# Performance work log

Hardware: AMD Instinct MI355X
Metric: run time of the kernel (lower is better)

## Reference

```python
import jax, jax.numpy as jnp
import numpy as np

V, E, H2, B, T, OUT = 50000, 300, 512, 32, 512, 256
H = H2 // 2  # hidden per direction


def _rand_mask(key, lengths, n_true):
    # exactly n_true True positions per row, all within the valid prefix [0, len)
    t = jnp.arange(T)[None, :]
    r = jax.random.uniform(key, (B, T)) + (t >= lengths[:, None]) * 10.0
    idx = jnp.argsort(r, axis=1)[:, :n_true]
    mask = jnp.zeros((B, T), dtype=bool)
    return mask.at[jnp.arange(B)[:, None], idx].set(True)


def setup_inputs() -> dict:
    key = jax.random.key(0)
    ks = jax.random.split(key, 12)
    inputs = jax.random.randint(ks[0], (B, T), 0, V)
    lengths = jnp.sort(jax.random.randint(ks[1], (B,), OUT, T + 1))[::-1]
    lengths = lengths.at[0].set(T)  # max length == padded length
    fmask = _rand_mask(ks[2], lengths, OUT)
    bmask = _rand_mask(ks[3], lengths, OUT)
    emb_scale = np.sqrt(3.0 / E).astype(np.float32)
    emb = jax.random.uniform(ks[4], (V, E), minval=-emb_scale, maxval=emb_scale, dtype=jnp.float32)
    k = 1.0 / np.sqrt(H).astype(np.float32)
    def u(kk, shape):
        return jax.random.uniform(kk, shape, minval=-k, maxval=k, dtype=jnp.float32)
    return {
        'inputs': inputs, 'seq_length': lengths, 'fmask': fmask, 'bmask': bmask,
        'out_seq_length': OUT, 'emb': emb,
        'W_ih_f': u(ks[5], (4 * H, E)), 'W_hh_f': u(ks[6], (4 * H, H)),
        'b_ih_f': u(ks[7], (4 * H,)), 'b_hh_f': u(ks[8], (4 * H,)),
        'W_ih_b': u(ks[9], (4 * H, E)), 'W_hh_b': u(ks[10], (4 * H, H)),
        'b_ih_b': u(ks[11], (4 * H,)), 'b_hh_b': u(ks[7], (4 * H,)),
    }


def run_lstm(xe, W_ih, W_hh, b_ih, b_hh):
    # PyTorch LSTM cell, gate order i,f,g,o. xe: (B,T,E) -> (B,T,H)
    xg = jnp.einsum('bte,ge->btg', xe, W_ih) + (b_ih + b_hh)
    def step(carry, xg_t):
        h, c = carry
        g = xg_t + h @ W_hh.T
        i, f, gg, o = jnp.split(g, 4, axis=-1)
        c = jax.nn.sigmoid(f) * c + jax.nn.sigmoid(i) * jnp.tanh(gg)
        h = jax.nn.sigmoid(o) * jnp.tanh(c)
        return (h, c), h
    h0 = jnp.zeros((xe.shape[0], W_hh.shape[1]), xe.dtype)
    _, hs = jax.lax.scan(step, (h0, h0), xg.transpose(1, 0, 2))
    return hs.transpose(1, 0, 2)


def select_masked(x, mask, out_len):
    # masked_select row-major order == indices of True in increasing t
    idx = jnp.argsort(jnp.logical_not(mask), axis=1, stable=True)[:, :out_len]
    return jnp.take_along_axis(x, idx[:, :, None], axis=1)


def reference(inputs, seq_length, fmask, bmask, out_seq_length, emb,
              W_ih_f, W_hh_f, b_ih_f, b_hh_f, W_ih_b, W_hh_b, b_ih_b, b_hh_b):
    t = jnp.arange(inputs.shape[1])[None, :]          # (1,T)
    valid = t < seq_length[:, None]                   # (B,T)
    # forward direction (dropout is identity at inference)
    f_out = run_lstm(emb[inputs], W_ih_f, W_hh_f, b_ih_f, b_hh_f)
    f_out = f_out * valid[..., None]                  # pad_packed zeros beyond len
    fsel = select_masked(f_out, fmask, out_seq_length)
    # per-batch sequence reversal of valid prefix (padding stays in place)
    rev_idx = jnp.where(valid, seq_length[:, None] - 1 - t, t)
    rinputs = jnp.take_along_axis(inputs, rev_idx, axis=1)
    b_out = run_lstm(emb[rinputs], W_ih_b, W_hh_b, b_ih_b, b_hh_b)
    b_out = b_out * valid[..., None]
    bsel = select_masked(b_out, bmask, out_seq_length)
    # re-reverse selected backward outputs per batch
    k = jnp.minimum(seq_length, out_seq_length)[:, None]
    t2 = jnp.arange(out_seq_length)[None, :]
    idx2 = jnp.where(t2 < k, out_seq_length - 1 - t2, t2 - k)
    bsel = jnp.take_along_axis(bsel, idx2[:, :, None], axis=1)
    return jnp.concatenate([fsel, bsel], axis=2)      # (B,out_seq,2H)
```

## Files before the change

### kernel.cpp

```cpp
#include <hip/hip_runtime.h>
#include <hip/hip_bf16.h>

#define B_   32
#define T_   512
#define E_   300
#define H_   256
#define OUT_ 256
#define ECH  100
#define GROWP 293

typedef unsigned long long u64;

__global__ __launch_bounds__(64) void slots_kernel(
    const unsigned char* __restrict__ fm, const unsigned char* __restrict__ bm,
    int* __restrict__ fslot, int* __restrict__ bpos)
{
    __shared__ unsigned char fL[B_ * T_];
    __shared__ unsigned char bL[B_ * T_];
    const int tid = threadIdx.x;

    const unsigned int* fw = (const unsigned int*)fm;
    int cnt = 0;
    for (int i = tid; i < 128; i += 64) {
        unsigned int v = fw[i];
        cnt += ((v & 0xFFu) != 0) + ((v & 0xFF00u) != 0)
             + ((v & 0xFF0000u) != 0) + ((v >> 24) != 0);
    }
#pragma unroll
    for (int off = 32; off; off >>= 1) cnt += __shfl_down(cnt, off, 64);
    bool isbool = __shfl(cnt, 0, 64) > 128;

    if (isbool) {
        for (int i = tid; i < B_ * T_ / 4; i += 64) {
            ((unsigned int*)fL)[i] = ((const unsigned int*)fm)[i];
            ((unsigned int*)bL)[i] = ((const unsigned int*)bm)[i];
        }
    } else {
        const unsigned int* bw = (const unsigned int*)bm;
        for (int i = tid; i < B_ * T_; i += 64) {
            fL[i] = fw[i] != 0;
            bL[i] = bw[i] != 0;
        }
    }
    __syncthreads();

    if (tid < B_) {
        int jf = 0, jb = 0;
        for (int t = 0; t < T_; ++t) {
            bool f = fL[tid * T_ + t] != 0;
            bool g = bL[tid * T_ + t] != 0;
            fslot[tid * T_ + t] = f ? (jf++) : -1;
            bpos [tid * T_ + t] = g ? (OUT_ - 1 - (jb++)) : -1;
        }
    }
}

__global__ __launch_bounds__(256) void xg_gemm(
    const int* __restrict__ inputs, const int* __restrict__ seqlen,
    const float* __restrict__ emb,
    const float* __restrict__ Wihf, const float* __restrict__ Wihb,
    const float* __restrict__ bihf, const float* __restrict__ bhhf,
    const float* __restrict__ bihb, const float* __restrict__ bhhb,
    float* __restrict__ xg, int t0, int TcMax)
{
    const int tg   = blockIdx.y;
    const int dir  = blockIdx.z;
    const int rblk = blockIdx.x * 64;
    const int tid  = threadIdx.x;

    __shared__ float eL[4][B_][ECH];
    __shared__ int   tokS[4][B_];

    if (tid < 128) {
        int t4 = tid >> 5, b = tid & 31;
        int t = t0 + tg * 4 + t4;
        int L = seqlen[b];
        int tt = t;
        if (dir) tt = (t < L) ? (L - 1 - t) : t;
        tokS[t4][b] = inputs[b * T_ + tt];
    }

    const float* W = dir ? Wihb : Wihf;
    const int b  = tid & 31;
    const int r8 = tid >> 5;

    float acc[4][8];
#pragma unroll
    for (int t4 = 0; t4 < 4; ++t4)
#pragma unroll
        for (int m = 0; m < 8; ++m) acc[t4][m] = 0.f;

    for (int ec = 0; ec < 3; ++ec) {
        __syncthreads();
        for (int idx = tid; idx < 3200; idx += 256) {
            int q  = idx % 25;
            int bb = (idx / 25) & 31;
            int t4 = idx / (25 * 32);
            const float* erow = emb + (size_t)tokS[t4][bb] * E_ + ec * ECH;
            *(float4*)&eL[t4][bb][q * 4] = *(const float4*)(erow + q * 4);
        }
        __syncthreads();

        for (int e4 = 0; e4 < 25; ++e4) {
            float4 w4[8];
#pragma unroll
            for (int m = 0; m < 8; ++m)
                w4[m] = *(const float4*)(W + (size_t)(rblk + r8 + m * 8) * E_
                                         + ec * ECH + e4 * 4);
#pragma unroll
            for (int t4 = 0; t4 < 4; ++t4) {
                float4 h4 = *(const float4*)&eL[t4][b][e4 * 4];
#pragma unroll
                for (int m = 0; m < 8; ++m)
                    acc[t4][m] += h4.x * w4[m].x + h4.y * w4[m].y
                                + h4.z * w4[m].z + h4.w * w4[m].w;
            }
        }
    }

    const float* bi = dir ? bihb : bihf;
    const float* bh = dir ? bhhb : bhhf;
#pragma unroll
    for (int t4 = 0; t4 < 4; ++t4) {
        float* outp = xg + (size_t)(dir * TcMax + tg * 4 + t4) * (1024 * B_);
#pragma unroll
        for (int m = 0; m < 8; ++m) {
            int row = rblk + r8 + m * 8;
            outp[(size_t)row * B_ + b] = acc[t4][m] + bi[row] + bh[row];
        }
    }
}

__global__ __launch_bounds__(512, 2) void fused_lstm(
    const int* __restrict__ inputs, const int* __restrict__ seqlen,
    const float* __restrict__ emb,
    const float* __restrict__ Wihf, const float* __restrict__ Whhf,
    const float* __restrict__ bihf, const float* __restrict__ bhhf,
    const float* __restrict__ Wihb, const float* __restrict__ Whhb,
    const float* __restrict__ bihb, const float* __restrict__ bhhb,
    const int* __restrict__ fslot, const int* __restrict__ bpos,
    u64* __restrict__ hbuf, float* __restrict__ cbuf,
    int* __restrict__ xgcnt, float* __restrict__ xg, float* __restrict__ out,
    int t0, int Tc, int fused)
{
    const int wg  = blockIdx.x;
    const int tid = threadIdx.x;
    __shared__ __align__(16) float smem[13824];

    if (wg >= 128) {
        float* eL   = smem;
        int*   tokS = (int*)(smem + 12800);
        const int hw = wg - 128;

        for (int j = hw; j < 2048; j += 128) {
            const int tg  = j >> 4;
            const int dir = (j >> 3) & 1;
            const int rp  = j & 7;
            const int rblk = (rp * 2 + (tid >> 8)) * 64;

            if (tid < 128) {
                int t4 = tid >> 5, b = tid & 31;
                int t = tg * 4 + t4;
                int L = seqlen[b];
                int tt = t;
                if (dir) tt = (t < L) ? (L - 1 - t) : t;
                tokS[t4 * B_ + b] = inputs[b * T_ + tt];
            }

            const float* W  = dir ? Wihb : Wihf;
            const int ltid = tid & 255;
            const int b  = ltid & 31;
            const int r8 = ltid >> 5;

            float acc[4][8];
#pragma unroll
            for (int t4 = 0; t4 < 4; ++t4)
#pragma unroll
                for (int m = 0; m < 8; ++m) acc[t4][m] = 0.f;

            for (int ec = 0; ec < 3; ++ec) {
                __syncthreads();
                for (int idx = tid; idx < 3200; idx += 512) {
                    int q  = idx % 25;
                    int bb = (idx / 25) & 31;
                    int t4 = idx / (25 * 32);
                    const float* erow = emb + (size_t)tokS[t4 * B_ + bb] * E_ + ec * ECH;
                    *(float4*)&eL[(t4 * B_ + bb) * ECH + q * 4] = *(const float4*)(erow + q * 4);
                }
                __syncthreads();

                for (int e4 = 0; e4 < 25; ++e4) {
                    float4 w4[8];
#pragma unroll
                    for (int m = 0; m < 8; ++m)
                        w4[m] = *(const float4*)(W + (size_t)(rblk + r8 + m * 8) * E_
                                                 + ec * ECH + e4 * 4);
#pragma unroll
                    for (int t4 = 0; t4 < 4; ++t4) {
                        float4 h4 = *(const float4*)&eL[(t4 * B_ + b) * ECH + e4 * 4];
#pragma unroll
                        for (int m = 0; m < 8; ++m)
                            acc[t4][m] += h4.x * w4[m].x + h4.y * w4[m].y
                                        + h4.z * w4[m].z + h4.w * w4[m].w;
                    }
                }
            }

            const float* bi = dir ? bihb : bihf;
            const float* bh = dir ? bhhb : bhhf;
#pragma unroll
            for (int t4 = 0; t4 < 4; ++t4) {
                float* outp = xg + (size_t)(dir * 512 + tg * 4 + t4) * (1024 * B_);
#pragma unroll
                for (int m = 0; m < 8; ++m) {
                    int row = rblk + r8 + m * 8;
                    __hip_atomic_store(&outp[(size_t)row * B_ + b],
                                       acc[t4][m] + bi[row] + bh[row],
                                       __ATOMIC_RELAXED, __HIP_MEMORY_SCOPE_AGENT);
                }
            }
            __syncthreads();
            if (tid == 0)
                __hip_atomic_fetch_add(&xgcnt[dir * 128 + tg], 1,
                                       __ATOMIC_RELAXED, __HIP_MEMORY_SCOPE_AGENT);
        }
        return;
    }

    float* hP   = smem;
    float* gbuf = smem + 8704;
    int*   sL   = (int*)(smem + 8704 + 4688);

    const int dir = wg >> 6;
    const int wgd = wg & 63;
    const int u0  = wgd * 4;

    const int rg  = tid & 3;
    const int bgr = (tid >> 2) & 7;
    const int kq  = tid >> 5;

    const float* Whh = dir ? Whhb : Whhf;

    float w[4][16];
#pragma unroll
    for (int r = 0; r < 4; ++r) {
        const float* wr = Whh + (size_t)(rg * H_ + u0 + r) * H_ + kq * 16;
#pragma unroll
        for (int q = 0; q < 4; ++q) {
            float4 v = *(const float4*)(wr + q * 4);
            w[r][q * 4 + 0] = v.x; w[r][q * 4 + 1] = v.y;
            w[r][q * 4 + 2] = v.z; w[r][q * 4 + 3] = v.w;
        }
    }
    if (tid < B_) sL[tid] = seqlen[tid];
    __syncthreads();

    const int ul = (tid >> 5) & 3, bb = tid & 31;
    float c_reg = 0.f;
    if (t0 > 0 && tid < 128)
        c_reg = cbuf[(size_t)(dir * 64 + wgd) * 128 + ul * 32 + bb];

    if (fused) {
        if (tid == 0) {
            const int* xc = xgcnt + dir * 128 + (t0 >> 2);
            while (__hip_atomic_load(xc, __ATOMIC_RELAXED,
                                     __HIP_MEMORY_SCOPE_AGENT) < 8)
                __builtin_amdgcn_s_sleep(1);
        }
        __syncthreads();
    }
    float xv0 = 0.f, xv1 = 0.f, xv2 = 0.f, xv3 = 0.f;
    float ya0 = 0.f, ya1 = 0.f, ya2 = 0.f, ya3 = 0.f;
    if (tid < 128) {
        const float* xp = xg + (size_t)(dir * Tc) * 32768 + (u0 + ul) * 32 + bb;
        xv0 = __hip_atomic_load(xp,         __ATOMIC_RELAXED, __HIP_MEMORY_SCOPE_AGENT);
        xv1 = __hip_atomic_load(xp +  8192, __ATOMIC_RELAXED, __HIP_MEMORY_SCOPE_AGENT);
        xv2 = __hip_atomic_load(xp + 16384, __ATOMIC_RELAXED, __HIP_MEMORY_SCOPE_AGENT);
        xv3 = __hip_atomic_load(xp + 24576, __ATOMIC_RELAXED, __HIP_MEMORY_SCOPE_AGENT);
        if (Tc > 1) {
            const float* xq = xp + 32768;
            ya0 = __hip_atomic_load(xq,         __ATOMIC_RELAXED, __HIP_MEMORY_SCOPE_AGENT);
            ya1 = __hip_atomic_load(xq +  8192, __ATOMIC_RELAXED, __HIP_MEMORY_SCOPE_AGENT);
            ya2 = __hip_atomic_load(xq + 16384, __ATOMIC_RELAXED, __HIP_MEMORY_SCOPE_AGENT);
            ya3 = __hip_atomic_load(xq + 24576, __ATOMIC_RELAXED, __HIP_MEMORY_SCOPE_AGENT);
        }
    }

    for (int tc = 0; tc < Tc; ++tc) {
        const int t = t0 + tc;

        if (t > 0) {
            const u64* hp = hbuf + (size_t)(dir * 2 + ((t - 1) & 1)) * 8192;
            u64 hr[16];
            for (;;) {
#pragma unroll
                for (int i = 0; i < 16; ++i)
                    hr[i] = __hip_atomic_load(hp + tid + 512 * i, __ATOMIC_RELAXED,
                                              __HIP_MEMORY_SCOPE_AGENT);
                bool ok = true;
#pragma unroll
                for (int i = 0; i < 16; ++i)
                    ok &= ((unsigned)(hr[i] >> 32) == (unsigned)t);
                if (__all(ok)) break;
                __builtin_amdgcn_s_sleep(1);
            }
#pragma unroll
            for (int i = 0; i < 16; ++i) {
                int wdx = tid + 512 * i;
                int k = ((wdx >> 7) << 2) | ((wdx >> 5) & 3);
                int b = wdx & 31;
                hP[((k >> 4) * 8 + (b >> 2)) * 68 + (k & 15) * 4 + (b & 3)] =
                    __uint_as_float((unsigned)hr[i]);
            }
        }
        __syncthreads();

        int cnt = 8;
        if (fused && tc + 2 < Tc && tid < 128)
            cnt = __hip_atomic_load(xgcnt + dir * 128 + ((t0 + tc + 2) >> 2),
                                    __ATOMIC_RELAXED, __HIP_MEMORY_SCOPE_AGENT);

        float acc[4][4];
#pragma unroll
        for (int r = 0; r < 4; ++r)
#pragma unroll
            for (int bi = 0; bi < 4; ++bi) acc[r][bi] = 0.f;

        if (t > 0) {
            const float* hblk = &hP[(kq * 8 + bgr) * 68];
#pragma unroll
            for (int kk = 0; kk < 16; ++kk) {
                float4 h4 = *(const float4*)(hblk + kk * 4);
#pragma unroll
                for (int r = 0; r < 4; ++r) {
                    acc[r][0] += w[r][kk] * h4.x;
                    acc[r][1] += w[r][kk] * h4.y;
                    acc[r][2] += w[r][kk] * h4.z;
                    acc[r][3] += w[r][kk] * h4.w;
                }
            }
        }

#pragma unroll
        for (int r = 0; r < 4; ++r)
#pragma unroll
            for (int bi = 0; bi < 4; ++bi)
                acc[r][bi] += __shfl_xor(acc[r][bi], 32, 64);

        if (((tid >> 5) & 1) == 0) {
            const int kq2 = kq >> 1;
#pragma unroll
            for (int r = 0; r < 4; ++r)
#pragma unroll
                for (int bi = 0; bi < 4; ++bi)
                    gbuf[(r * 4 + rg) * GROWP + (bgr * 4 + bi) * 9 + kq2] = acc[r][bi];
        }
        __syncthreads();

        float hnew = 0.f;
        float* oaddr = nullptr;
        if (tid < 128) {
            const int u = u0 + ul;
            if (t < sL[bb]) {
                float gi = xv0, gf = xv1, gg = xv2, go = xv3;
#pragma unroll
                for (int q = 0; q < 8; ++q) {
                    gi += gbuf[(ul * 4 + 0) * GROWP + bb * 9 + q];
                    gf += gbuf[(ul * 4 + 1) * GROWP + bb * 9 + q];
                    gg += gbuf[(ul * 4 + 2) * GROWP + bb * 9 + q];
                    go += gbuf[(ul * 4 + 3) * GROWP + bb * 9 + q];
                }
                float si = 1.f / (1.f + expf(-gi));
                float sf = 1.f / (1.f + expf(-gf));
                float so = 1.f / (1.f + expf(-go));
                c_reg = sf * c_reg + si * tanhf(gg);
                hnew  = so * tanhf(c_reg);
                if (dir == 0) {
                    int j = fslot[bb * T_ + t];
                    if (j >= 0) oaddr = &out[((size_t)bb * OUT_ + j) * 512 + u];
                } else {
                    int p = bpos[bb * T_ + t];
                    if (p >= 0) oaddr = &out[((size_t)bb * OUT_ + p) * 512 + 256 + u];
                }
            } else {
                hnew = hP[((u >> 4) * 8 + (bb >> 2)) * 68 + (u & 15) * 4 + (bb & 3)];
            }
            u64 pkt = ((u64)(unsigned)(t + 1) << 32) | (u64)__float_as_uint(hnew);
            u64* hn = hbuf + (size_t)(dir * 2 + (t & 1)) * 8192;
            __hip_atomic_store(&hn[wgd * 128 + tid], pkt,
                               __ATOMIC_RELAXED, __HIP_MEMORY_SCOPE_AGENT);
        }
        __syncthreads();

        float z0 = 0.f, z1 = 0.f, z2 = 0.f, z3 = 0.f;
        if (tc + 2 < Tc && tid < 128) {
            if (fused && cnt < 8) {
                const int* xc = xgcnt + dir * 128 + ((t0 + tc + 2) >> 2);
                while (__hip_atomic_load(xc, __ATOMIC_RELAXED,
                                         __HIP_MEMORY_SCOPE_AGENT) < 8)
                    __builtin_amdgcn_s_sleep(1);
            }
            const float* xp = xg + (size_t)(dir * Tc + tc + 2) * 32768 + (u0 + ul) * 32 + bb;
            z0 = __hip_atomic_load(xp,         __ATOMIC_RELAXED, __HIP_MEMORY_SCOPE_AGENT);
            z1 = __hip_atomic_load(xp +  8192, __ATOMIC_RELAXED, __HIP_MEMORY_SCOPE_AGENT);
            z2 = __hip_atomic_load(xp + 16384, __ATOMIC_RELAXED, __HIP_MEMORY_SCOPE_AGENT);
            z3 = __hip_atomic_load(xp + 24576, __ATOMIC_RELAXED, __HIP_MEMORY_SCOPE_AGENT);
        }
        if (oaddr)
            __hip_atomic_store(oaddr, hnew, __ATOMIC_RELAXED,
                               __HIP_MEMORY_SCOPE_AGENT);
        xv0 = ya0; xv1 = ya1; xv2 = ya2; xv3 = ya3;
        ya0 = z0;  ya1 = z1;  ya2 = z2;  ya3 = z3;
    }

    if (tid < 128)
        cbuf[(size_t)(dir * 64 + wgd) * 128 + ul * 32 + bb] = c_reg;
}

extern "C" void kernel_launch(void* const* d_in, const int* in_sizes, int n_in,
                              void* d_out, int out_size, void* d_ws, size_t ws_size,
                              hipStream_t stream) {
    const int*           inputs = (const int*)d_in[0];
    const int*           seqlen = (const int*)d_in[1];
    const unsigned char* fm     = (const unsigned char*)d_in[2];
    const unsigned char* bm     = (const unsigned char*)d_in[3];
    const float* emb  = (const float*)d_in[5];
    const float* Wihf = (const float*)d_in[6];
    const float* Whhf = (const float*)d_in[7];
    const float* bihf = (const float*)d_in[8];
    const float* bhhf = (const float*)d_in[9];
    const float* Wihb = (const float*)d_in[10];
    const float* Whhb = (const float*)d_in[11];
    const float* bihb = (const float*)d_in[12];
    const float* bhhb = (const float*)d_in[13];
    float* out = (float*)d_out;

    char* ws = (char*)d_ws;
    int*   fslot = (int*)(ws);
    int*   bpos  = (int*)(ws + 65536);
    u64*   hbuf  = (u64*)(ws + 131072);
    float* cbuf  = (float*)(ws + 393216);
    int*   xgcnt = (int*)(ws + 458752);
    float* xg    = (float*)(ws + 460800);
    (void)in_sizes; (void)n_in; (void)out_size;

    size_t avail = (ws_size > 460800) ? ws_size - 460800 : 0;
    int Tc = 4;
    for (int c = 512; c >= 4; c >>= 1)
        if ((size_t)c * 262144 <= avail) { Tc = c; break; }

    (void)hipMemsetAsync(ws + 131072, 0, 262144, stream);
    (void)hipMemsetAsync(ws + 458752, 0, 1024, stream);
    slots_kernel<<<1, 64, 0, stream>>>(fm, bm, fslot, bpos);

    if (Tc == 512) {
        fused_lstm<<<256, 512, 0, stream>>>(
            inputs, seqlen, emb, Wihf, Whhf, bihf, bhhf,
            Wihb, Whhb, bihb, bhhb, fslot, bpos,
            hbuf, cbuf, xgcnt, xg, out, 0, 512, 1);
    } else {
        for (int t0 = 0; t0 < T_; t0 += Tc) {
            dim3 g(16, Tc / 4, 2);
            xg_gemm<<<g, 256, 0, stream>>>(inputs, seqlen, emb, Wihf, Wihb,
                                           bihf, bhhf, bihb, bhhb, xg, t0, Tc);
            fused_lstm<<<128, 512, 0, stream>>>(
                inputs, seqlen, emb, Wihf, Whhf, bihf, bhhf,
                Wihb, Whhb, bihb, bhhb, fslot, bpos,
                hbuf, cbuf, xgcnt, xg, out, t0, Tc, 0);
        }
    }
}
```

Baseline: 1.998 ms.

## Poll only stale hidden-state slots and drop trailing per-step barrier

The spin-wait on the shared hidden-state buffer now re-loads only the slots whose step tag is still stale, instead of re-reading all 16 each iteration. For padded timesteps the previous hidden value is kept in a register (h_own), seeded from hbuf at chunk start, rather than read back from shared memory. That removes the dependence on hP and allows the trailing __syncthreads after the gate/publish stage to be removed. The xg prefetch and output store now live inside the tid<128 branch. This trims barrier and polling traffic on the serial per-step critical path, but relies on the next iteration's barrier to order gbuf/hP reuse.

```diff
diff --git a/kernel.cpp b/kernel.cpp
--- a/kernel.cpp
+++ b/kernel.cpp
@@ -257,8 +257,14 @@
 
     const int ul = (tid >> 5) & 3, bb = tid & 31;
     float c_reg = 0.f;
-    if (t0 > 0 && tid < 128)
+    float h_own = 0.f;
+    if (t0 > 0 && tid < 128) {
         c_reg = cbuf[(size_t)(dir * 64 + wgd) * 128 + ul * 32 + bb];
+        u64 p = __hip_atomic_load(
+            hbuf + (size_t)(dir * 2 + ((t0 - 1) & 1)) * 8192 + wgd * 128 + tid,
+            __ATOMIC_RELAXED, __HIP_MEMORY_SCOPE_AGENT);
+        h_own = __uint_as_float((unsigned)p);
+    }
 
     if (fused) {
         if (tid == 0) {
@@ -292,17 +298,23 @@
         if (t > 0) {
             const u64* hp = hbuf + (size_t)(dir * 2 + ((t - 1) & 1)) * 8192;
             u64 hr[16];
+#pragma unroll
+            for (int i = 0; i < 16; ++i)
+                hr[i] = __hip_atomic_load(hp + tid + 512 * i, __ATOMIC_RELAXED,
+                                          __HIP_MEMORY_SCOPE_AGENT);
             for (;;) {
+                unsigned bad = 0;
 #pragma unroll
                 for (int i = 0; i < 16; ++i)
-                    hr[i] = __hip_atomic_load(hp + tid + 512 * i, __ATOMIC_RELAXED,
-                                              __HIP_MEMORY_SCOPE_AGENT);
-                bool ok = true;
+                    if ((unsigned)(hr[i] >> 32) != (unsigned)t) bad |= (1u << i);
+                if (__all(bad == 0)) break;
+                __builtin_amdgcn_s_sleep(1);
 #pragma unroll
                 for (int i = 0; i < 16; ++i)
-                    ok &= ((unsigned)(hr[i] >> 32) == (unsigned)t);
-                if (__all(ok)) break;
-                __builtin_amdgcn_s_sleep(1);
+                    if (bad & (1u << i))
+                        hr[i] = __hip_atomic_load(hp + tid + 512 * i,
+                                                  __ATOMIC_RELAXED,
+                                                  __HIP_MEMORY_SCOPE_AGENT);
             }
 #pragma unroll
             for (int i = 0; i < 16; ++i) {
@@ -357,10 +369,10 @@
         }
         __syncthreads();
 
-        float hnew = 0.f;
-        float* oaddr = nullptr;
         if (tid < 128) {
             const int u = u0 + ul;
+            float hnew;
+            float* oaddr = nullptr;
             if (t < sL[bb]) {
                 float gi = xv0, gf = xv1, gg = xv2, go = xv3;
 #pragma unroll
@@ -383,34 +395,35 @@
                     if (p >= 0) oaddr = &out[((size_t)bb * OUT_ + p) * 512 + 256 + u];
                 }
             } else {
-                hnew = hP[((u >> 4) * 8 + (bb >> 2)) * 68 + (u & 15) * 4 + (bb & 3)];
-            }
+                hnew = h_own;
+            }
+            h_own = hnew;
             u64 pkt = ((u64)(unsigned)(t + 1) << 32) | (u64)__float_as_uint(hnew);
             u64* hn = hbuf + (size_t)(dir * 2 + (t & 1)) * 8192;
             __hip_atomic_store(&hn[wgd * 128 + tid], pkt,
                                __ATOMIC_RELAXED, __HIP_MEMORY_SCOPE_AGENT);
-        }
-        __syncthreads();
-
-        float z0 = 0.f, z1 = 0.f, z2 = 0.f, z3 = 0.f;
-        if (tc + 2 < Tc && tid < 128) {
-            if (fused && cnt < 8) {
-                const int* xc = xgcnt + dir * 128 + ((t0 + tc + 2) >> 2);
-                while (__hip_atomic_load(xc, __ATOMIC_RELAXED,
-                                         __HIP_MEMORY_SCOPE_AGENT) < 8)
-                    __builtin_amdgcn_s_sleep(1);
-            }
-            const float* xp = xg + (size_t)(dir * Tc + tc + 2) * 32768 + (u0 + ul) * 32 + bb;
-            z0 = __hip_atomic_load(xp,         __ATOMIC_RELAXED, __HIP_MEMORY_SCOPE_AGENT);
-            z1 = __hip_atomic_load(xp +  8192, __ATOMIC_RELAXED, __HIP_MEMORY_SCOPE_AGENT);
-            z2 = __hip_atomic_load(xp + 16384, __ATOMIC_RELAXED, __HIP_MEMORY_SCOPE_AGENT);
-            z3 = __hip_atomic_load(xp + 24576, __ATOMIC_RELAXED, __HIP_MEMORY_SCOPE_AGENT);
-        }
-        if (oaddr)
-            __hip_atomic_store(oaddr, hnew, __ATOMIC_RELAXED,
-                               __HIP_MEMORY_SCOPE_AGENT);
-        xv0 = ya0; xv1 = ya1; xv2 = ya2; xv3 = ya3;
-        ya0 = z0;  ya1 = z1;  ya2 = z2;  ya3 = z3;
+
+            if (oaddr)
+                __hip_atomic_store(oaddr, hnew, __ATOMIC_RELAXED,
+                                   __HIP_MEMORY_SCOPE_AGENT);
+            float z0 = 0.f, z1 = 0.f, z2 = 0.f, z3 = 0.f;
+            if (tc + 2 < Tc) {
+                if (fused && cnt < 8) {
+                    const int* xc = xgcnt + dir * 128 + ((t0 + tc + 2) >> 2);
+                    while (__hip_atomic_load(xc, __ATOMIC_RELAXED,
+                                             __HIP_MEMORY_SCOPE_AGENT) < 8)
+                        __builtin_amdgcn_s_sleep(1);
+                }
+                const float* xp = xg + (size_t)(dir * Tc + tc + 2) * 32768
+                                  + (u0 + ul) * 32 + bb;
+                z0 = __hip_atomic_load(xp,         __ATOMIC_RELAXED, __HIP_MEMORY_SCOPE_AGENT);
+                z1 = __hip_atomic_load(xp +  8192, __ATOMIC_RELAXED, __HIP_MEMORY_SCOPE_AGENT);
+                z2 = __hip_atomic_load(xp + 16384, __ATOMIC_RELAXED, __HIP_MEMORY_SCOPE_AGENT);
+                z3 = __hip_atomic_load(xp + 24576, __ATOMIC_RELAXED, __HIP_MEMORY_SCOPE_AGENT);
+            }
+            xv0 = ya0; xv1 = ya1; xv2 = ya2; xv3 = ya3;
+            ya0 = z0;  ya1 = z1;  ya2 = z2;  ya3 = z3;
+        }
     }
 
     if (tid < 128)
```

Result: slower. 2.253 ms (+12.7%).
